# Kernel optimization log

Hardware: AMD Instinct MI355X
Metric: run time of the kernel (lower is better)

## Reference

```python
import jax, jax.numpy as jnp
import numpy as np

D_MODEL = 1024
N_HEAD = 16


def setup_inputs() -> dict:
    key = jax.random.key(0)
    k1, k2, k3 = jax.random.split(key, 3)
    scale = 1.0 / np.sqrt(D_MODEL)
    x = jax.random.normal(k1, (1, 4096, D_MODEL), dtype=jnp.float32)
    # nn.Linear weights stored as [out, in]; applied as x @ W.T
    w_attn = jax.random.normal(k2, (3 * D_MODEL, D_MODEL), dtype=jnp.float32) * scale
    w_proj = jax.random.normal(k3, (D_MODEL, D_MODEL), dtype=jnp.float32) * scale
    return {"x": x, "w_attn": w_attn, "w_proj": w_proj}


def reference(x, w_attn, w_proj):
    B, T, C = x.shape
    H = N_HEAD
    hd = C // H
    qkv = x @ w_attn.T                      # [B, T, 3C]
    q, k, v = jnp.split(qkv, 3, axis=-1)
    # [B, T, C] -> [B, H, T, hd]
    q = q.reshape(B, T, H, hd).transpose(0, 2, 1, 3)
    k = k.reshape(B, T, H, hd).transpose(0, 2, 1, 3)
    v = v.reshape(B, T, H, hd).transpose(0, 2, 1, 3)
    att = jnp.einsum("bhqd,bhkd->bhqk", q, k) * (1.0 / np.sqrt(hd))  # [B,H,T,T]
    causal = jnp.tril(jnp.ones((T, T), dtype=bool))
    att = jnp.where(causal[None, None], att, -jnp.inf)
    att = jax.nn.softmax(att, axis=-1)
    y = jnp.einsum("bhqk,bhkd->bhqd", att, v)  # [B,H,T,hd]
    y = y.transpose(0, 2, 1, 3).reshape(B, T, C)
    return y @ w_proj.T
```

## Files before the change

### kernel.cpp

```cpp
#include <hip/hip_runtime.h>
#include <hip/hip_bf16.h>
#include <stdint.h>

typedef __bf16 bf16x8 __attribute__((ext_vector_type(8)));
typedef float f32x4 __attribute__((ext_vector_type(4)));

#define T_SEQ 4096
#define C_DIM 1024
#define H_NUM 16
#define HD 64
#define C3 3072
#define NEG_BIG (-30000.0f)

__device__ __forceinline__ unsigned short f2bf(float f) {
    uint32_t u = __builtin_bit_cast(uint32_t, f);
    u += 0x7fffu + ((u >> 16) & 1u);
    return (unsigned short)(u >> 16);
}

__device__ __forceinline__ uint32_t pk_bf16(float a, float b) {
    __hip_bfloat162 h = __float22bfloat162_rn(float2{a, b});
    uint32_t u;
    __builtin_memcpy(&u, &h, sizeof(u));
    return u;
}

__device__ __forceinline__ bf16x8 ld_bf8(const unsigned short* p) {
    return *reinterpret_cast<const bf16x8*>(p);
}

__device__ __forceinline__ void async_g2l16(const unsigned short* g, unsigned short* l) {
    __builtin_amdgcn_global_load_lds(
        (const __attribute__((address_space(1))) void*)g,
        (__attribute__((address_space(3))) void*)l, 16, 0, 0);
}

__device__ __forceinline__ void store_c(unsigned short* C, size_t idx, float v) { C[idx] = f2bf(v); }
__device__ __forceinline__ void store_c(float* C, size_t idx, float v)          { C[idx] = v; }

__device__ __forceinline__ void cvt8(const float* src, unsigned short* dst) {
    float4 f0 = *(const float4*)src;
    float4 f1 = *(const float4*)(src + 4);
    union { uint32_t w[4]; uint4 q; } t;
    t.w[0] = pk_bf16(f0.x, f0.y);
    t.w[1] = pk_bf16(f0.z, f0.w);
    t.w[2] = pk_bf16(f1.x, f1.y);
    t.w[3] = pk_bf16(f1.z, f1.w);
    *(uint4*)dst = t.q;
}

__global__ void cvt_xw(const float* __restrict__ x, const float* __restrict__ wa,
                       unsigned short* __restrict__ xb, unsigned short* __restrict__ wab) {
    int i = (blockIdx.x * blockDim.x + threadIdx.x) * 8;
    if (i < T_SEQ * C_DIM) cvt8(x + i, xb + i);
    else {
        int k = i - T_SEQ * C_DIM;
        if (k < C3 * C_DIM) cvt8(wa + k, wab + k);
    }
}

__global__ void cvt_f32_bf16(const float* __restrict__ src, unsigned short* __restrict__ dst, int n) {
    int i = (blockIdx.x * blockDim.x + threadIdx.x) * 8;
    if (i >= n) return;
    cvt8(src + i, dst + i);
}

__global__ __launch_bounds__(256) void v_transpose(
    const unsigned short* __restrict__ qkv, unsigned short* __restrict__ Vt)
{
    __shared__ unsigned short tile[64][72];
    const int t0 = blockIdx.x * 64, c0 = blockIdx.y * 64;
    const int r = threadIdx.x >> 2, q = threadIdx.x & 3;

    const unsigned short* src = qkv + (size_t)(t0 + r) * C3 + 2 * C_DIM + c0 + q * 16;
    *(uint4*)&tile[r][q * 16]     = *(const uint4*)src;
    *(uint4*)&tile[r][q * 16 + 8] = *(const uint4*)(src + 8);
    __syncthreads();

    union { unsigned short u[16]; uint4 v[2]; } o;
    #pragma unroll
    for (int j = 0; j < 16; ++j) o.u[j] = tile[q * 16 + j][r];
    unsigned short* dst = Vt + (size_t)(c0 + r) * T_SEQ + t0 + q * 16;
    *(uint4*)dst       = o.v[0];
    *(uint4*)(dst + 8) = o.v[1];
}

template <typename TC>
__global__ __launch_bounds__(256, 2) void gemm_bt(
    const unsigned short* __restrict__ A, const unsigned short* __restrict__ B,
    TC* __restrict__ C, int M, int N, int K)
{
    __shared__ __attribute__((aligned(16))) unsigned short As[128 * 32];
    __shared__ __attribute__((aligned(16))) unsigned short Bs[128 * 32];

    const int tid  = threadIdx.x;
    const int wave = tid >> 6, lane = tid & 63;
    const int quad = lane >> 4, l16 = lane & 15;
    const int wm = wave >> 1, wn = wave & 1;
    const int m0 = blockIdx.y * 128, n0 = blockIdx.x * 128;

    const int srow = wave * 32 + (lane >> 2);
    const int scol = (lane & 3) * 8;

    f32x4 acc[4][4] = {};

    for (int k0 = 0; k0 < K; k0 += 32) {
        {
            const unsigned short* ga = A + (size_t)(m0 + srow) * K + k0 + scol;
            const unsigned short* gb = B + (size_t)(n0 + srow) * K + k0 + scol;
            unsigned short* la = As + (wave * 32) * 32;
            unsigned short* lb = Bs + (wave * 32) * 32;
            async_g2l16(ga, la);
            async_g2l16(ga + (size_t)16 * K, la + 16 * 32);
            async_g2l16(gb, lb);
            async_g2l16(gb + (size_t)16 * K, lb + 16 * 32);
        }
        __syncthreads();

        bf16x8 af[4], bf[4];
        #pragma unroll
        for (int i = 0; i < 4; ++i) {
            af[i] = ld_bf8(As + (wm * 64 + i * 16 + l16) * 32 + quad * 8);
            bf[i] = ld_bf8(Bs + (wn * 64 + i * 16 + l16) * 32 + quad * 8);
        }
        #pragma unroll
        for (int mt = 0; mt < 4; ++mt)
            #pragma unroll
            for (int nt = 0; nt < 4; ++nt)
                acc[mt][nt] = __builtin_amdgcn_mfma_f32_16x16x32_bf16(
                    af[mt], bf[nt], acc[mt][nt], 0, 0, 0);
        __syncthreads();
    }

    #pragma unroll
    for (int mt = 0; mt < 4; ++mt)
        #pragma unroll
        for (int nt = 0; nt < 4; ++nt)
            #pragma unroll
            for (int r = 0; r < 4; ++r) {
                int row = m0 + wm * 64 + mt * 16 + quad * 4 + r;
                int col = n0 + wn * 64 + nt * 16 + l16;
                store_c(C, (size_t)row * N + col, acc[mt][nt][r]);
            }
}

template <bool MASK>
__device__ __forceinline__ void fa8_tile(
    const unsigned short* Ksb, const unsigned short* Vsb, unsigned short* pbuf,
    const bf16x8 qf[2][2], f32x4 o[2][4], float* l_part,
    int k0, int q_abs0, int quad, int l16, int sw, int fo0, int fo1)
{
    const unsigned short* krow = Ksb + l16 * 64;
    bf16x8 kf[4][2];
    #pragma unroll
    for (int s = 0; s < 4; ++s) {
        kf[s][0] = ld_bf8(krow + s * 1024 + fo0);
        kf[s][1] = ld_bf8(krow + s * 1024 + fo1);
    }

    #pragma unroll
    for (int qs = 0; qs < 2; ++qs) {
        f32x4 st[4];
        #pragma unroll
        for (int s = 0; s < 4; ++s) {
            f32x4 z = {};
            z = __builtin_amdgcn_mfma_f32_16x16x32_bf16(kf[s][0], qf[qs][0], z, 0, 0, 0);
            st[s] = __builtin_amdgcn_mfma_f32_16x16x32_bf16(kf[s][1], qf[qs][1], z, 0, 0, 0);
        }
        float ts = 0.f;
        #pragma unroll
        for (int s = 0; s < 4; ++s)
            #pragma unroll
            for (int r = 0; r < 4; ++r) {
                float v = st[s][r];
                if (MASK) {
                    int key = k0 + s * 16 + quad * 4 + r;
                    v = (key <= q_abs0 + qs * 16) ? v : NEG_BIG;
                }
                float e = __builtin_amdgcn_exp2f(v);
                st[s][r] = e;
                ts += e;
            }
        l_part[qs] += ts;

        unsigned short* prow = pbuf + (qs * 16 + l16) * 64;
        #pragma unroll
        for (int s = 0; s < 4; ++s) {
            int g = 2 * s + (quad >> 1);
            uint2 pk;
            pk.x = pk_bf16(st[s][0], st[s][1]);
            pk.y = pk_bf16(st[s][2], st[s][3]);
            *(uint2*)((char*)prow + (g ^ sw) * 16 + 8 * (quad & 1)) = pk;
        }
    }

    const unsigned short* vrow = Vsb + l16 * 64;
    bf16x8 vf[4][2];
    #pragma unroll
    for (int c = 0; c < 4; ++c) {
        vf[c][0] = ld_bf8(vrow + c * 1024 + fo0);
        vf[c][1] = ld_bf8(vrow + c * 1024 + fo1);
    }
    #pragma unroll
    for (int qs = 0; qs < 2; ++qs) {
        const unsigned short* prow = pbuf + (qs * 16 + l16) * 64;
        bf16x8 pf0 = ld_bf8(prow + fo0);
        bf16x8 pf1 = ld_bf8(prow + fo1);
        #pragma unroll
        for (int c = 0; c < 4; ++c) {
            o[qs][c] = __builtin_amdgcn_mfma_f32_16x16x32_bf16(vf[c][0], pf0, o[qs][c], 0, 0, 0);
            o[qs][c] = __builtin_amdgcn_mfma_f32_16x16x32_bf16(vf[c][1], pf1, o[qs][c], 0, 0, 0);
        }
    }
}

__global__ __launch_bounds__(256, 3) void flash_attn8(
    const unsigned short* __restrict__ qkv,
    const unsigned short* __restrict__ Vt,
    unsigned short* __restrict__ Y)
{
    __shared__ __attribute__((aligned(16))) unsigned short Ks[2][64 * 64];
    __shared__ __attribute__((aligned(16))) unsigned short Vs[2][64 * 64];
    __shared__ __attribute__((aligned(16))) unsigned short Pl[4][32 * 64];

    const int tid  = threadIdx.x;
    const int wave = tid >> 6, lane = tid & 63;
    const int quad = lane >> 4, l16 = lane & 15;

    const int bi = blockIdx.x;
    const int rr = bi >> 8, ss = bi & 255;
    const int h  = ss & 15;
    const int j  = ss >> 4;
    const int qb = rr ? (31 - j) : j;

    const int q0w    = qb * 128 + wave * 32;
    const int q_abs0 = q0w + l16;
    const int sw  = l16 & 7;
    const int fo0 = (quad ^ sw) * 8;
    const int fo1 = ((quad + 4) ^ sw) * 8;

    bf16x8 qf[2][2];
    {
        const float QS = 0.125f * 1.44269504f;
        #pragma unroll
        for (int qs = 0; qs < 2; ++qs) {
            const unsigned short* qp =
                qkv + (size_t)(q0w + qs * 16 + l16) * C3 + h * HD + quad * 8;
            bf16x8 a = ld_bf8(qp), b = ld_bf8(qp + 32);
            #pragma unroll
            for (int i = 0; i < 8; ++i) {
                qf[qs][0][i] = (__bf16)((float)a[i] * QS);
                qf[qs][1][i] = (__bf16)((float)b[i] * QS);
            }
        }
    }

    const int srow = lane >> 3;
    const int schunk = (lane & 7) ^ srow;
    const unsigned short* kp0 =
        qkv + (size_t)(wave * 16 + srow) * C3 + C_DIM + h * HD + schunk * 8;
    const unsigned short* kp1 = kp0 + (size_t)8 * C3;
    const unsigned short* vp0 =
        Vt + (size_t)(h * HD + wave * 16 + srow) * T_SEQ + schunk * 8;
    const unsigned short* vp1 = vp0 + (size_t)8 * T_SEQ;
    unsigned short* lk0  = Ks[0] + (wave * 16) * 64;
    unsigned short* lk0b = lk0 + 8 * 64;
    unsigned short* lv0  = Vs[0] + (wave * 16) * 64;
    unsigned short* lv0b = lv0 + 8 * 64;
    const int lds_db = 64 * 64;

    f32x4 o[2][4] = {};
    float l_part[2] = {0.f, 0.f};
    unsigned short* pbuf = Pl[wave];

    const int ntiles = 2 * qb + 2;
    const int mask_t = 2 * qb + (wave >> 1);

    async_g2l16(kp0, lk0);  async_g2l16(kp1, lk0b);
    async_g2l16(vp0, lv0);  async_g2l16(vp1, lv0b);
    kp0 += (size_t)64 * C3; kp1 += (size_t)64 * C3;
    vp0 += 64;              vp1 += 64;

    for (int t = 0; t < ntiles; ++t) {
        __syncthreads();
        const int b = t & 1;
        if (t + 1 < ntiles) {
            const int nb = 1 - b;
            async_g2l16(kp0, lk0 + nb * lds_db);
            async_g2l16(kp1, lk0b + nb * lds_db);
            async_g2l16(vp0, lv0 + nb * lds_db);
            async_g2l16(vp1, lv0b + nb * lds_db);
            kp0 += (size_t)64 * C3; kp1 += (size_t)64 * C3;
            vp0 += 64;              vp1 += 64;
        }
        if (t < mask_t) {
            fa8_tile<false>(Ks[b], Vs[b], pbuf, qf, o, l_part,
                            t * 64, q_abs0, quad, l16, sw, fo0, fo1);
        } else if (t == mask_t) {
            fa8_tile<true>(Ks[b], Vs[b], pbuf, qf, o, l_part,
                           t * 64, q_abs0, quad, l16, sw, fo0, fo1);
        }
    }

    #pragma unroll
    for (int qs = 0; qs < 2; ++qs) {
        float l = l_part[qs];
        l += __shfl_xor(l, 16, 64);
        l += __shfl_xor(l, 32, 64);
        float inv_l = 1.f / l;
        #pragma unroll
        for (int c = 0; c < 4; ++c) {
            union { uint32_t w[2]; uint2 q; } t;
            t.w[0] = pk_bf16(o[qs][c][0] * inv_l, o[qs][c][1] * inv_l);
            t.w[1] = pk_bf16(o[qs][c][2] * inv_l, o[qs][c][3] * inv_l);
            *(uint2*)(Y + (size_t)(q_abs0 + qs * 16) * C_DIM + h * HD + c * 16 + quad * 4) = t.q;
        }
    }
}

extern "C" void kernel_launch(void* const* d_in, const int* in_sizes, int n_in,
                              void* d_out, int out_size, void* d_ws, size_t ws_size,
                              hipStream_t stream) {
    const float* x      = (const float*)d_in[0];
    const float* w_attn = (const float*)d_in[1];
    const float* w_proj = (const float*)d_in[2];
    float* out = (float*)d_out;

    unsigned short* qkv = (unsigned short*)d_ws;
    unsigned short* xb  = qkv + (size_t)T_SEQ * C3;
    unsigned short* y   = xb;
    unsigned short* wpb = qkv;
    unsigned short* Vt  = (unsigned short*)d_out;
    unsigned short* wab = Vt + (size_t)C_DIM * T_SEQ;

    cvt_xw<<<(T_SEQ * C_DIM + C3 * C_DIM) / 8 / 256, 256, 0, stream>>>(x, w_attn, xb, wab);

    gemm_bt<unsigned short>
        <<<dim3(C3 / 128, T_SEQ / 128), 256, 0, stream>>>(xb, wab, qkv, T_SEQ, C3, C_DIM);

    v_transpose<<<dim3(T_SEQ / 64, C_DIM / 64), 256, 0, stream>>>(qkv, Vt);

    flash_attn8<<<dim3(512), 256, 0, stream>>>(qkv, Vt, y);

    cvt_f32_bf16<<<(C_DIM * C_DIM / 8 + 255) / 256, 256, 0, stream>>>(w_proj, wpb, C_DIM * C_DIM);
    gemm_bt<float>
        <<<dim3(C_DIM / 128, T_SEQ / 128), 256, 0, stream>>>(y, wpb, out, T_SEQ, C_DIM, C_DIM);
}
```

Before: 220.8 us.

## Compute V transposed via GEMM, fuse weight conversions, load V fragments from global

Result: slower. 312.0 us (+41.3%).

```diff
diff --git a/kernel.cpp b/kernel.cpp
--- a/kernel.cpp
+++ b/kernel.cpp
@@ -10,6 +10,7 @@
 #define H_NUM 16
 #define HD 64
 #define C3 3072
+#define QKS 2048
 #define NEG_BIG (-30000.0f)
 
 __device__ __forceinline__ unsigned short f2bf(float f) {
@@ -49,40 +50,18 @@
     *(uint4*)dst = t.q;
 }
 
-__global__ void cvt_xw(const float* __restrict__ x, const float* __restrict__ wa,
-                       unsigned short* __restrict__ xb, unsigned short* __restrict__ wab) {
+#define XN (T_SEQ * C_DIM)
+#define WAN (C3 * C_DIM)
+#define WPN (C_DIM * C_DIM)
+
+__global__ void cvt_all(const float* __restrict__ x, const float* __restrict__ wa,
+                        const float* __restrict__ wp,
+                        unsigned short* __restrict__ xb, unsigned short* __restrict__ wab,
+                        unsigned short* __restrict__ wpb) {
     int i = (blockIdx.x * blockDim.x + threadIdx.x) * 8;
-    if (i < T_SEQ * C_DIM) cvt8(x + i, xb + i);
-    else {
-        int k = i - T_SEQ * C_DIM;
-        if (k < C3 * C_DIM) cvt8(wa + k, wab + k);
-    }
-}
-
-__global__ void cvt_f32_bf16(const float* __restrict__ src, unsigned short* __restrict__ dst, int n) {
-    int i = (blockIdx.x * blockDim.x + threadIdx.x) * 8;
-    if (i >= n) return;
-    cvt8(src + i, dst + i);
-}
-
-__global__ __launch_bounds__(256) void v_transpose(
-    const unsigned short* __restrict__ qkv, unsigned short* __restrict__ Vt)
-{
-    __shared__ unsigned short tile[64][72];
-    const int t0 = blockIdx.x * 64, c0 = blockIdx.y * 64;
-    const int r = threadIdx.x >> 2, q = threadIdx.x & 3;
-
-    const unsigned short* src = qkv + (size_t)(t0 + r) * C3 + 2 * C_DIM + c0 + q * 16;
-    *(uint4*)&tile[r][q * 16]     = *(const uint4*)src;
-    *(uint4*)&tile[r][q * 16 + 8] = *(const uint4*)(src + 8);
-    __syncthreads();
-
-    union { unsigned short u[16]; uint4 v[2]; } o;
-    #pragma unroll
-    for (int j = 0; j < 16; ++j) o.u[j] = tile[q * 16 + j][r];
-    unsigned short* dst = Vt + (size_t)(c0 + r) * T_SEQ + t0 + q * 16;
-    *(uint4*)dst       = o.v[0];
-    *(uint4*)(dst + 8) = o.v[1];
+    if (i < XN) cvt8(x + i, xb + i);
+    else if (i < XN + WAN) { int k = i - XN; cvt8(wa + k, wab + k); }
+    else { int k = i - XN - WAN; if (k < WPN) cvt8(wp + k, wpb + k); }
 }
 
 template <typename TC>
@@ -145,8 +124,8 @@
 }
 
 template <bool MASK>
-__device__ __forceinline__ void fa8_tile(
-    const unsigned short* Ksb, const unsigned short* Vsb, unsigned short* pbuf,
+__device__ __forceinline__ void fa9_tile(
+    const unsigned short* Ksb, const bf16x8 vf[4][2], unsigned short* pbuf,
     const bf16x8 qf[2][2], f32x4 o[2][4], float* l_part,
     int k0, int q_abs0, int quad, int l16, int sw, int fo0, int fo1)
 {
@@ -194,13 +173,6 @@
         }
     }
 
-    const unsigned short* vrow = Vsb + l16 * 64;
-    bf16x8 vf[4][2];
-    #pragma unroll
-    for (int c = 0; c < 4; ++c) {
-        vf[c][0] = ld_bf8(vrow + c * 1024 + fo0);
-        vf[c][1] = ld_bf8(vrow + c * 1024 + fo1);
-    }
     #pragma unroll
     for (int qs = 0; qs < 2; ++qs) {
         const unsigned short* prow = pbuf + (qs * 16 + l16) * 64;
@@ -214,13 +186,12 @@
     }
 }
 
-__global__ __launch_bounds__(256, 3) void flash_attn8(
-    const unsigned short* __restrict__ qkv,
+__global__ __launch_bounds__(256, 3) void flash_attn9(
+    const unsigned short* __restrict__ qk,
     const unsigned short* __restrict__ Vt,
     unsigned short* __restrict__ Y)
 {
     __shared__ __attribute__((aligned(16))) unsigned short Ks[2][64 * 64];
-    __shared__ __attribute__((aligned(16))) unsigned short Vs[2][64 * 64];
     __shared__ __attribute__((aligned(16))) unsigned short Pl[4][32 * 64];
 
     const int tid  = threadIdx.x;
@@ -245,7 +216,7 @@
         #pragma unroll
         for (int qs = 0; qs < 2; ++qs) {
             const unsigned short* qp =
-                qkv + (size_t)(q0w + qs * 16 + l16) * C3 + h * HD + quad * 8;
+                qk + (size_t)(q0w + qs * 16 + l16) * QKS + h * HD + quad * 8;
             bf16x8 a = ld_bf8(qp), b = ld_bf8(qp + 32);
             #pragma unroll
             for (int i = 0; i < 8; ++i) {
@@ -258,16 +229,13 @@
     const int srow = lane >> 3;
     const int schunk = (lane & 7) ^ srow;
     const unsigned short* kp0 =
-        qkv + (size_t)(wave * 16 + srow) * C3 + C_DIM + h * HD + schunk * 8;
-    const unsigned short* kp1 = kp0 + (size_t)8 * C3;
-    const unsigned short* vp0 =
-        Vt + (size_t)(h * HD + wave * 16 + srow) * T_SEQ + schunk * 8;
-    const unsigned short* vp1 = vp0 + (size_t)8 * T_SEQ;
+        qk + (size_t)(wave * 16 + srow) * QKS + C_DIM + h * HD + schunk * 8;
+    const unsigned short* kp1 = kp0 + (size_t)8 * QKS;
     unsigned short* lk0  = Ks[0] + (wave * 16) * 64;
     unsigned short* lk0b = lk0 + 8 * 64;
-    unsigned short* lv0  = Vs[0] + (wave * 16) * 64;
-    unsigned short* lv0b = lv0 + 8 * 64;
     const int lds_db = 64 * 64;
+
+    const unsigned short* vb = Vt + (size_t)(h * HD + l16) * T_SEQ + quad * 8;
 
     f32x4 o[2][4] = {};
     float l_part[2] = {0.f, 0.f};
@@ -277,28 +245,37 @@
     const int mask_t = 2 * qb + (wave >> 1);
 
     async_g2l16(kp0, lk0);  async_g2l16(kp1, lk0b);
-    async_g2l16(vp0, lv0);  async_g2l16(vp1, lv0b);
-    kp0 += (size_t)64 * C3; kp1 += (size_t)64 * C3;
-    vp0 += 64;              vp1 += 64;
+    kp0 += (size_t)64 * QKS; kp1 += (size_t)64 * QKS;
 
     for (int t = 0; t < ntiles; ++t) {
         __syncthreads();
         const int b = t & 1;
+        const bool active = (t <= mask_t);
+
+        bf16x8 vf[4][2];
+        if (active) {
+            const unsigned short* v0 = vb + t * 64;
+            #pragma unroll
+            for (int c = 0; c < 4; ++c) {
+                vf[c][0] = ld_bf8(v0 + (size_t)(c * 16) * T_SEQ);
+                vf[c][1] = ld_bf8(v0 + (size_t)(c * 16) * T_SEQ + 32);
+            }
+        }
+
         if (t + 1 < ntiles) {
             const int nb = 1 - b;
             async_g2l16(kp0, lk0 + nb * lds_db);
             async_g2l16(kp1, lk0b + nb * lds_db);
-            async_g2l16(vp0, lv0 + nb * lds_db);
-            async_g2l16(vp1, lv0b + nb * lds_db);
-            kp0 += (size_t)64 * C3; kp1 += (size_t)64 * C3;
-            vp0 += 64;              vp1 += 64;
-        }
-        if (t < mask_t) {
-            fa8_tile<false>(Ks[b], Vs[b], pbuf, qf, o, l_part,
-                            t * 64, q_abs0, quad, l16, sw, fo0, fo1);
-        } else if (t == mask_t) {
-            fa8_tile<true>(Ks[b], Vs[b], pbuf, qf, o, l_part,
-                           t * 64, q_abs0, quad, l16, sw, fo0, fo1);
+            kp0 += (size_t)64 * QKS; kp1 += (size_t)64 * QKS;
+        }
+
+        if (active) {
+            if (t < mask_t)
+                fa9_tile<false>(Ks[b], vf, pbuf, qf, o, l_part,
+                                t * 64, q_abs0, quad, l16, sw, fo0, fo1);
+            else
+                fa9_tile<true>(Ks[b], vf, pbuf, qf, o, l_part,
+                               t * 64, q_abs0, quad, l16, sw, fo0, fo1);
         }
     }
 
@@ -326,23 +303,24 @@
     const float* w_proj = (const float*)d_in[2];
     float* out = (float*)d_out;
 
-    unsigned short* qkv = (unsigned short*)d_ws;
-    unsigned short* xb  = qkv + (size_t)T_SEQ * C3;
+    unsigned short* qk  = (unsigned short*)d_ws;
+    unsigned short* xb  = qk + (size_t)T_SEQ * QKS;
     unsigned short* y   = xb;
-    unsigned short* wpb = qkv;
+    unsigned short* wpb = xb + (size_t)T_SEQ * C_DIM;
     unsigned short* Vt  = (unsigned short*)d_out;
     unsigned short* wab = Vt + (size_t)C_DIM * T_SEQ;
-
-    cvt_xw<<<(T_SEQ * C_DIM + C3 * C_DIM) / 8 / 256, 256, 0, stream>>>(x, w_attn, xb, wab);
+    unsigned short* wvb = wab + (size_t)2048 * C_DIM;
+
+    cvt_all<<<(XN + WAN + WPN) / 8 / 256, 256, 0, stream>>>(x, w_attn, w_proj, xb, wab, wpb);
 
     gemm_bt<unsigned short>
-        <<<dim3(C3 / 128, T_SEQ / 128), 256, 0, stream>>>(xb, wab, qkv, T_SEQ, C3, C_DIM);
-
-    v_transpose<<<dim3(T_SEQ / 64, C_DIM / 64), 256, 0, stream>>>(qkv, Vt);
-
-    flash_attn8<<<dim3(512), 256, 0, stream>>>(qkv, Vt, y);
-
-    cvt_f32_bf16<<<(C_DIM * C_DIM / 8 + 255) / 256, 256, 0, stream>>>(w_proj, wpb, C_DIM * C_DIM);
+        <<<dim3(QKS / 128, T_SEQ / 128), 256, 0, stream>>>(xb, wab, qk, T_SEQ, QKS, C_DIM);
+
+    gemm_bt<unsigned short>
+        <<<dim3(T_SEQ / 128, C_DIM / 128), 256, 0, stream>>>(wvb, xb, Vt, C_DIM, T_SEQ, C_DIM);
+
+    flash_attn9<<<dim3(512), 256, 0, stream>>>(qk, Vt, y);
+
     gemm_bt<float>
         <<<dim3(C_DIM / 128, T_SEQ / 128), 256, 0, stream>>>(y, wpb, out, T_SEQ, C_DIM, C_DIM);
 }
```
